# Performance work log

Hardware: AMD Instinct MI355X
Metric: run time of the kernel (lower is better)

Reference implementation:

```python
import jax, jax.numpy as jnp
import numpy as np

D_MODEL = 2048
DOWN = 512
UP = 1024
NUM_HEADS = 16
ROPE_DIM = 64
BS = 16
SEQ = 512
BASE = 10000.0
HEAD_DIM = D_MODEL // NUM_HEADS          # 128 (used only in the softmax scale)
V_HEAD_DIM = UP // NUM_HEADS             # 64


def _linear(x, W, b):
    # torch nn.Linear: y = x @ W.T + b, W shape (out, in)
    return x @ W.T + b


def _rope(x, num_heads, rope_dim):
    # Faithful to source RotaryEmbedding, including the swapped sin/cos caches:
    #   cos_pos = sin(pos*theta), sin_pos = cos(pos*theta)
    bs, L, _ = x.shape
    q = x.reshape(bs, L, num_heads, rope_dim).transpose(0, 2, 1, 3)  # (bs,h,L,d)
    theta = 1.0 / (BASE ** (jnp.arange(0, rope_dim, 2, dtype=jnp.float32) / rope_dim))
    ang = jnp.arange(L, dtype=jnp.float32)[:, None] * theta[None, :]   # (L, d/2)
    cos_pos = jnp.repeat(jnp.sin(ang), 2, axis=-1)  # (L, d) -- source quirk
    sin_pos = jnp.repeat(jnp.cos(ang), 2, axis=-1)
    q2 = jnp.stack([-q[..., 1::2], q[..., ::2]], axis=-1).reshape(bs, num_heads, L, rope_dim)
    return q * cos_pos + q2 * sin_pos


def setup_inputs() -> dict:
    key = jax.random.key(0)
    ks = jax.random.split(key, 18)
    s = 0.02
    d = {
        "h": jax.random.normal(ks[0], (BS, SEQ, D_MODEL), jnp.float32),
        "W_down_kv": jax.random.normal(ks[1], (DOWN, D_MODEL), jnp.float32) * s,
        "b_down_kv": jnp.zeros((DOWN,), jnp.float32),
        "W_up_k": jax.random.normal(ks[2], (UP, DOWN), jnp.float32) * s,
        "b_up_k": jnp.zeros((UP,), jnp.float32),
        "W_up_v": jax.random.normal(ks[3], (UP, DOWN), jnp.float32) * s,
        "b_up_v": jnp.zeros((UP,), jnp.float32),
        "W_down_q": jax.random.normal(ks[4], (DOWN, D_MODEL), jnp.float32) * s,
        "b_down_q": jnp.zeros((DOWN,), jnp.float32),
        "W_up_q": jax.random.normal(ks[5], (UP, DOWN), jnp.float32) * s,
        "b_up_q": jnp.zeros((UP,), jnp.float32),
        "W_qr": jax.random.normal(ks[6], (ROPE_DIM * NUM_HEADS, DOWN), jnp.float32) * s,
        "b_qr": jnp.zeros((ROPE_DIM * NUM_HEADS,), jnp.float32),
        "W_kr": jax.random.normal(ks[7], (ROPE_DIM, D_MODEL), jnp.float32) * s,
        "b_kr": jnp.zeros((ROPE_DIM,), jnp.float32),
        "W_fc": jax.random.normal(ks[8], (D_MODEL, NUM_HEADS * V_HEAD_DIM), jnp.float32) * s,
        "b_fc": jnp.zeros((D_MODEL,), jnp.float32),
    }
    return d


def reference(h, W_down_kv, b_down_kv, W_up_k, b_up_k, W_up_v, b_up_v,
              W_down_q, b_down_q, W_up_q, b_up_q, W_qr, b_qr,
              W_kr, b_kr, W_fc, b_fc):
    bs, L, _ = h.shape
    # low-rank KV path
    c_kv = _linear(h, W_down_kv, b_down_kv)             # (bs,L,down)
    k_c = _linear(c_kv, W_up_k, b_up_k)                 # (bs,L,up)
    v_c = _linear(c_kv, W_up_v, b_up_v)                 # (bs,L,up)
    # low-rank Q path
    c_q = _linear(h, W_down_q, b_down_q)                # (bs,L,down)
    q_c = _linear(c_q, W_up_q, b_up_q)                  # (bs,L,up)
    # rope (decoupled) path
    q_r = _rope(_linear(c_q, W_qr, b_qr), NUM_HEADS, ROPE_DIM)  # (bs,H,L,rope)
    k_r = _rope(_linear(h, W_kr, b_kr), 1, ROPE_DIM)            # (bs,1,L,rope)

    q_c = q_c.reshape(bs, L, NUM_HEADS, -1).transpose(0, 2, 1, 3)  # (bs,H,L,64)
    q = jnp.concatenate([q_c, q_r], axis=-1)                        # (bs,H,L,128)
    k_c = k_c.reshape(bs, L, NUM_HEADS, -1).transpose(0, 2, 1, 3)
    k_r = jnp.broadcast_to(k_r, (bs, NUM_HEADS, L, ROPE_DIM))       # shared across heads
    k = jnp.concatenate([k_c, k_r], axis=-1)

    scale = 1.0 / jnp.sqrt(jnp.float32(HEAD_DIM + ROPE_DIM))  # sqrt(192), per source
    scores = jnp.einsum('bhqd,bhkd->bhqk', q, k) * scale
    attn = jax.nn.softmax(scores, axis=-1)  # dropout is identity in eval mode

    v = v_c.reshape(bs, L, NUM_HEADS, V_HEAD_DIM).transpose(0, 2, 1, 3)
    out = jnp.einsum('bhqk,bhkd->bhqd', attn, v)
    out = out.transpose(0, 2, 1, 3).reshape(bs, L, -1)   # (bs,L,H*v_head_dim)
    return _linear(out, W_fc, b_fc)                      # (bs,L,d_model)
```

## Files before the change

kernel.cpp:

```cpp
#include <hip/hip_runtime.h>
#include <hip/hip_bf16.h>

typedef __bf16 bf16x8 __attribute__((ext_vector_type(8)));
typedef float f32x4 __attribute__((ext_vector_type(4)));
using u16 = unsigned short;
using u32 = unsigned int;

__device__ __forceinline__ float bf2f(u16 v) {
    unsigned int u = (unsigned int)v << 16;
    float f; __builtin_memcpy(&f, &u, 4); return f;
}
__device__ __forceinline__ u16 f2bf(float f) {
    unsigned int u; __builtin_memcpy(&u, &f, 4);
    u += 0x7FFFu + ((u >> 16) & 1u);
    return (u16)(u >> 16);
}

struct Cvt9 {
    const float* src[9];
    u16* dst[9];
    int end[9];
};
__global__ __launch_bounds__(256) void cvt_all(Cvt9 d, int total)
{
    int c = blockIdx.x * 256 + threadIdx.x;
    if (c >= total) return;
    int seg = 0;
    while (c >= d.end[seg]) ++seg;
    int local = c - (seg ? d.end[seg - 1] : 0);
    const float* s = d.src[seg] + (size_t)local * 8;
    float4 f0 = *(const float4*)s;
    float4 f1 = *(const float4*)(s + 4);
    u16 tmp[8] = { f2bf(f0.x), f2bf(f0.y), f2bf(f0.z), f2bf(f0.w),
                   f2bf(f1.x), f2bf(f1.y), f2bf(f1.z), f2bf(f1.w) };
    *(uint4*)(d.dst[seg] + (size_t)local * 8) = *(const uint4*)tmp;
}

struct Cpy7 {
    const float* src[7];
    float* dst[7];
    int end[7];
};
__global__ __launch_bounds__(256) void copy_f32(Cpy7 d, int total)
{
    int c = blockIdx.x * 256 + threadIdx.x;
    if (c >= total) return;
    int seg = 0;
    while (c >= d.end[seg]) ++seg;
    int local = c - (seg ? d.end[seg - 1] : 0);
    d.dst[seg][local] = d.src[seg][local];
}

template<bool CF>
__global__ __launch_bounds__(256) void gemm_v5(
    const u16* __restrict__ A0, const u16* __restrict__ B0, void* __restrict__ C0, const float* __restrict__ e0,
    const u16* __restrict__ A1, const u16* __restrict__ B1, void* __restrict__ C1, const float* __restrict__ e1,
    int ysplit, int lda, int ldb, int ldc, int N, int K)
{
    __shared__ __align__(16) u16 As[3][128 * 32];
    __shared__ __align__(16) u16 Bs[3][128 * 32];

    const int t = threadIdx.x;
    const int lane = t & 63;
    const int w = t >> 6;
    const int wm = w >> 1, wn = w & 1;
    const int l16 = lane & 15, quad = lane >> 4;
    const int m0 = blockIdx.x * 128;

    const u16* A; const u16* B; void* Cv; const float* bias; int yl;
    if ((int)blockIdx.y < ysplit) { A = A0; B = B0; Cv = C0; bias = e0; yl = blockIdx.y; }
    else                          { A = A1; B = B1; Cv = C1; bias = e1; yl = blockIdx.y - ysplit; }
    const int n0 = yl * 128;

    const int sub  = lane >> 2;
    const int slot = lane & 3;
    const int agc  = slot ^ ((sub >> 1) & 3);
    const int sfr  = (l16 >> 1) & 3;

    f32x4 acc[4][4];
#pragma unroll
    for (int i = 0; i < 4; ++i)
#pragma unroll
        for (int j = 0; j < 4; ++j) acc[i][j] = (f32x4){0.f, 0.f, 0.f, 0.f};

    auto STAGE = [&](int buf, int k0) {
#pragma unroll
        for (int c = 0; c < 2; ++c) {
            const int rr = w * 32 + c * 16;
            const u16* ga = A + (size_t)(m0 + rr + sub) * lda + k0 + agc * 8;
            __builtin_amdgcn_global_load_lds(
                (const __attribute__((address_space(1))) u32*)ga,
                (__attribute__((address_space(3))) u32*)&As[buf][rr * 32], 16, 0, 0);
            const u16* gb = B + (size_t)(n0 + rr + sub) * ldb + k0 + agc * 8;
            __builtin_amdgcn_global_load_lds(
                (const __attribute__((address_space(1))) u32*)gb,
                (__attribute__((address_space(3))) u32*)&Bs[buf][rr * 32], 16, 0, 0);
        }
    };

    const int nt = K >> 5;
    STAGE(0, 0);
    STAGE(1, 32);
    int cur = 0;
    for (int tt = 0; tt < nt; ++tt) {
        int pre = cur + 2; if (pre >= 3) pre -= 3;
        if (tt + 2 < nt) {
            STAGE(pre, (tt + 2) << 5);
            asm volatile("s_waitcnt vmcnt(8)");
        } else if (tt + 1 < nt) {
            asm volatile("s_waitcnt vmcnt(4)");
        } else {
            asm volatile("s_waitcnt vmcnt(0)");
        }
        __builtin_amdgcn_sched_barrier(0);
        __builtin_amdgcn_s_barrier();
        __builtin_amdgcn_sched_barrier(0);

        const u16* Ab = As[cur];
        const u16* Bb = Bs[cur];
        bf16x8 af[4], bfr[4];
#pragma unroll
        for (int i = 0; i < 4; ++i)
            af[i] = *(const bf16x8*)&Ab[(wm * 64 + i * 16 + l16) * 32 + (quad ^ sfr) * 8];
#pragma unroll
        for (int j = 0; j < 4; ++j)
            bfr[j] = *(const bf16x8*)&Bb[(wn * 64 + j * 16 + l16) * 32 + (quad ^ sfr) * 8];
#pragma unroll
        for (int i = 0; i < 4; ++i)
#pragma unroll
            for (int j = 0; j < 4; ++j)
                acc[i][j] = __builtin_amdgcn_mfma_f32_16x16x32_bf16(bfr[j], af[i], acc[i][j], 0, 0, 0);

        __builtin_amdgcn_s_barrier();
        __builtin_amdgcn_sched_barrier(0);
        cur += 1; if (cur >= 3) cur -= 3;
    }

#pragma unroll
    for (int i = 0; i < 4; ++i) {
        const int row = m0 + wm * 64 + i * 16 + l16;
#pragma unroll
        for (int j = 0; j < 4; ++j) {
            const int colb = n0 + wn * 64 + j * 16 + quad * 4;
            if (colb >= N) continue;
            float4 bv = *(const float4*)&bias[colb];
            float v0 = acc[i][j][0] + bv.x;
            float v1 = acc[i][j][1] + bv.y;
            float v2 = acc[i][j][2] + bv.z;
            float v3 = acc[i][j][3] + bv.w;
            if (CF) {
                float4 out = { v0, v1, v2, v3 };
                *(float4*)((float*)Cv + (size_t)row * ldc + colb) = out;
            } else {
                u16 p[4] = { f2bf(v0), f2bf(v1), f2bf(v2), f2bf(v3) };
                *(uint2*)((u16*)Cv + (size_t)row * ldc + colb) = *(const uint2*)p;
            }
        }
    }
}

__global__ void rope_inplace(u16* __restrict__ buf, int ld, int col0, int ppr, int total)
{
    int idx = blockIdx.x * 256 + threadIdx.x;
    if (idx >= total) return;
    int row = idx / ppr;
    int pi  = idx - row * ppr;
    int grp = pi >> 5;
    int i   = pi & 31;
    int pos = row & 511;
    float theta = __expf(-(float)i * 0.2878231366242558f);
    float ang = (float)pos * theta;
    float s = sinf(ang), c = cosf(ang);
    size_t base = (size_t)row * ld + col0 + grp * 64 + 2 * i;
    float x0 = bf2f(buf[base]);
    float x1 = bf2f(buf[base + 1]);
    buf[base]     = f2bf(x0 * s - x1 * c);
    buf[base + 1] = f2bf(x1 * s + x0 * c);
}

__global__ __launch_bounds__(256) void attn_kernel(
    const u16* __restrict__ q_src,
    const u16* __restrict__ kv_src,
    const u16* __restrict__ kr_src,
    u16* __restrict__ o_dst, int ldo)
{
    __shared__ __align__(16) u16 Ks[64 * 136];
    __shared__ __align__(16) u16 Vt[64 * 72];
    __shared__ __align__(16) u16 Ps[64 * 72];

    const int t = threadIdx.x;
    const int lane = t & 63;
    const int w = t >> 6;
    const int l16 = lane & 15, quad = lane >> 4;

    const int id   = blockIdx.x;
    const int xcd  = id & 7;
    const int qt   = (id >> 3) & 7;
    const int panel = xcd + ((id >> 6) << 3);
    const int h = panel & 15;
    const int b = panel >> 4;
    const int qrow0 = b * 512 + qt * 64;
    const int krow_base = b * 512;

    bf16x8 aq[4];
    {
        const u16* qrow = q_src + (size_t)(qrow0 + w * 16 + l16) * 2048;
#pragma unroll
        for (int ks = 0; ks < 4; ++ks) {
            int col = ks * 32 + quad * 8;
            const u16* src = (col < 64) ? qrow + h * 64 + col
                                        : qrow + 1024 + h * 64 + (col - 64);
            aq[ks] = *(const bf16x8*)src;
        }
    }

    const int colK = (t & 15) * 8;
    const int r0k  = t >> 4;
    const u16* kbase; int kstr;
    if (colK < 64) { kbase = kv_src + h * 64 + colK;        kstr = 2048; }
    else           { kbase = kr_src + 1024 + (colK - 64);   kstr = 1088; }
    u16* kw = &Ks[r0k * 136 + colK];

    const int v00 = (t & 7) * 8;
    const int r0v = t >> 3;
    const u16* vbase = kv_src + 1024 + h * 64 + v00;
    const int rotA = (r0v + v00) & 63;
    const int rotB = (r0v + 32 + v00) & 63;
    u16* vwA = &Vt[v00 * 72 + rotA];
    u16* vwB = &Vt[v00 * 72 + rotB];

    auto LOADT = [&](int krow0, uint4& K0, uint4& K1, uint4& K2, uint4& K3,
                     uint4& V0, uint4& V1) {
        K0 = *(const uint4*)(kbase + (size_t)(krow0 + r0k     ) * kstr);
        K1 = *(const uint4*)(kbase + (size_t)(krow0 + r0k + 16) * kstr);
        K2 = *(const uint4*)(kbase + (size_t)(krow0 + r0k + 32) * kstr);
        K3 = *(const uint4*)(kbase + (size_t)(krow0 + r0k + 48) * kstr);
        V0 = *(const uint4*)(vbase + (size_t)(krow0 + r0v     ) * 2048);
        V1 = *(const uint4*)(vbase + (size_t)(krow0 + r0v + 32) * 2048);
    };
    auto WRITET = [&](const uint4& K0, const uint4& K1, const uint4& K2, const uint4& K3,
                      const uint4& V0, const uint4& V1) {
        *(uint4*)(kw)            = K0;
        *(uint4*)(kw + 16 * 136) = K1;
        *(uint4*)(kw + 32 * 136) = K2;
        *(uint4*)(kw + 48 * 136) = K3;
        u16 ta[8], tb[8];
        __builtin_memcpy(ta, &V0, 16);
        __builtin_memcpy(tb, &V1, 16);
#pragma unroll
        for (int j2 = 0; j2 < 8; ++j2) { vwA[j2 * 72] = ta[j2]; vwB[j2 * 72] = tb[j2]; }
    };

    float m2[4], l_run[4];
    f32x4 o[4];
#pragma unroll
    for (int r = 0; r < 4; ++r) { m2[r] = -1e30f; l_run[r] = 0.f; }
#pragma unroll
    for (int n = 0; n < 4; ++n) o[n] = (f32x4){0.f, 0.f, 0.f, 0.f};

    const float C = 0.10411756f;
    const int Rp = (64 - (quad << 4)) & 48;
    const int Rr = (64 - ((l16 >> 2) << 4)) & 48;

    uint4 kA0, kA1, kA2, kA3, vA0, vA1;
    uint4 kB0, kB1, kB2, kB3, vB0, vB1;
    LOADT(krow_base, kA0, kA1, kA2, kA3, vA0, vA1);

    for (int kt = 0; kt < 8; ++kt) {
        __builtin_amdgcn_s_barrier();
        __builtin_amdgcn_sched_barrier(0);
        if ((kt & 1) == 0) {
            WRITET(kA0, kA1, kA2, kA3, vA0, vA1);
            if (kt < 7) LOADT(krow_base + (kt + 1) * 64, kB0, kB1, kB2, kB3, vB0, vB1);
        } else {
            WRITET(kB0, kB1, kB2, kB3, vB0, vB1);
            if (kt < 7) LOADT(krow_base + (kt + 1) * 64, kA0, kA1, kA2, kA3, vA0, vA1);
        }
        asm volatile("s_waitcnt lgkmcnt(0)");
        __builtin_amdgcn_sched_barrier(0);
        __builtin_amdgcn_s_barrier();
        __builtin_amdgcn_sched_barrier(0);

        f32x4 s[4];
#pragma unroll
        for (int n = 0; n < 4; ++n) s[n] = (f32x4){0.f, 0.f, 0.f, 0.f};
#pragma unroll
        for (int ks = 0; ks < 4; ++ks) {
#pragma unroll
            for (int n = 0; n < 4; ++n) {
                bf16x8 bk = *(const bf16x8*)&Ks[(n * 16 + l16) * 136 + ks * 32 + quad * 8];
                s[n] = __builtin_amdgcn_mfma_f32_16x16x32_bf16(aq[ks], bk, s[n], 0, 0, 0);
            }
        }

        float mx[4], alpha[4], rs[4];
#pragma unroll
        for (int r = 0; r < 4; ++r)
            mx[r] = fmaxf(fmaxf(s[0][r], s[1][r]), fmaxf(s[2][r], s[3][r]));
#pragma unroll
        for (int d = 1; d < 16; d <<= 1)
#pragma unroll
            for (int r = 0; r < 4; ++r)
                mx[r] = fmaxf(mx[r], __shfl_xor(mx[r], d));
#pragma unroll
        for (int r = 0; r < 4; ++r) {
            float mnew = fmaxf(m2[r], mx[r] * C);
            alpha[r] = __builtin_amdgcn_exp2f(m2[r] - mnew);
            m2[r] = mnew;
            rs[r] = 0.f;
#pragma unroll
            for (int n = 0; n < 4; ++n) {
                float pv = __builtin_amdgcn_exp2f(__builtin_fmaf(s[n][r], C, -mnew));
                s[n][r] = pv;
                rs[r] += pv;
            }
        }
#pragma unroll
        for (int d = 1; d < 16; d <<= 1)
#pragma unroll
            for (int r = 0; r < 4; ++r)
                rs[r] += __shfl_xor(rs[r], d);
#pragma unroll
        for (int r = 0; r < 4; ++r) {
            l_run[r] = l_run[r] * alpha[r] + rs[r];
#pragma unroll
            for (int n = 0; n < 4; ++n) o[n][r] *= alpha[r];
        }

#pragma unroll
        for (int n = 0; n < 4; ++n) {
            int pc = (n * 16 + l16 + Rp) & 63;
#pragma unroll
            for (int r = 0; r < 4; ++r)
                Ps[(w * 16 + quad * 4 + r) * 72 + pc] = f2bf(s[n][r]);
        }

#pragma unroll
        for (int kk = 0; kk < 2; ++kk) {
            bf16x8 ap = *(const bf16x8*)&Ps[(w * 16 + l16) * 72 + ((kk * 32 + quad * 8 + Rr) & 63)];
#pragma unroll
            for (int n = 0; n < 4; ++n) {
                bf16x8 bv = *(const bf16x8*)&Vt[(n * 16 + l16) * 72
                              + ((kk * 32 + quad * 8 + n * 16 + (l16 & 8)) & 63)];
                o[n] = __builtin_amdgcn_mfma_f32_16x16x32_bf16(ap, bv, o[n], 0, 0, 0);
            }
        }
    }

#pragma unroll
    for (int r = 0; r < 4; ++r) {
        float inv = 1.0f / l_run[r];
        int row = qrow0 + w * 16 + quad * 4 + r;
#pragma unroll
        for (int n = 0; n < 4; ++n) {
            int col = h * 64 + n * 16 + l16;
            o_dst[(size_t)row * ldo + col] = f2bf(o[n][r] * inv);
        }
    }
}

extern "C" void kernel_launch(void* const* d_in, const int* in_sizes, int n_in,
                              void* d_out, int out_size, void* d_ws, size_t ws_size,
                              hipStream_t stream)
{
    const float* h    = (const float*)d_in[0];
    const float* Wdkv = (const float*)d_in[1];
    const float* bdkv = (const float*)d_in[2];
    const float* Wuk  = (const float*)d_in[3];
    const float* buk  = (const float*)d_in[4];
    const float* Wuv  = (const float*)d_in[5];
    const float* buv  = (const float*)d_in[6];
    const float* Wdq  = (const float*)d_in[7];
    const float* bdq  = (const float*)d_in[8];
    const float* Wuq  = (const float*)d_in[9];
    const float* buq  = (const float*)d_in[10];
    const float* Wqr  = (const float*)d_in[11];
    const float* bqr  = (const float*)d_in[12];
    const float* Wkr  = (const float*)d_in[13];
    const float* bkr  = (const float*)d_in[14];
    const float* Wfc  = (const float*)d_in[15];
    const float* bfc  = (const float*)d_in[16];

    char* ws = (char*)d_ws;
    u16* out1   = (u16*)ws;
    u16* hbf    = (u16*)(ws + 17825792);
    u16* out2a  = hbf;
    u16* out2b  = (u16*)(ws + 51380224);
    u16* w1     = (u16*)(ws + 84934656);
    u16* w2a    = (u16*)(ws + 89653248);
    u16* w2b    = (u16*)(ws + 91750400);
    u16* wfc    = (u16*)(ws + 93847552);
    float* bias_s1 = (float*)(ws + 98041856);
    float* bias_2  = (float*)(ws + 98046208);

    Cvt9 cd;
    const float* srcs[9] = { h, Wdkv, Wdq, Wkr, Wuk, Wuv, Wuq, Wqr, Wfc };
    u16* dsts[9] = { hbf, w1, w1 + 512 * 2048, w1 + 1024 * 2048,
                     w2a, w2a + 1024 * 512, w2b, w2b + 1024 * 512, wfc };
    int cnts[9] = { 2097152, 131072, 131072, 16384, 65536, 65536, 65536, 65536, 262144 };
    int acc2 = 0;
    for (int i = 0; i < 9; ++i) { cd.src[i] = srcs[i]; cd.dst[i] = dsts[i]; acc2 += cnts[i]; cd.end[i] = acc2; }
    cvt_all<<<(acc2 + 255) / 256, 256, 0, stream>>>(cd, acc2);
    hipMemsetAsync(w1 + 1088 * 2048, 0, 64 * 2048 * sizeof(u16), stream);

    Cpy7 bc;
    const float* bs[7] = { bdkv, bdq, bkr, buk, buv, buq, bqr };
    float* bd[7] = { bias_s1, bias_s1 + 512, bias_s1 + 1024,
                     bias_2, bias_2 + 1024, bias_2 + 2048, bias_2 + 3072 };
    int bn[7] = { 512, 512, 64, 1024, 1024, 1024, 1024 };
    int bacc = 0;
    for (int i = 0; i < 7; ++i) { bc.src[i] = bs[i]; bc.dst[i] = bd[i]; bacc += bn[i]; bc.end[i] = bacc; }
    copy_f32<<<(bacc + 255) / 256, 256, 0, stream>>>(bc, bacc);

    gemm_v5<false><<<dim3(64, 9), 256, 0, stream>>>(
        hbf, w1, out1, bias_s1,
        hbf, w1, out1, bias_s1, 9, 2048, 2048, 1088, 1088, 2048);
    rope_inplace<<<1024, 256, 0, stream>>>(out1, 1088, 1024, 32, 8192 * 32);

    gemm_v5<false><<<dim3(64, 32), 256, 0, stream>>>(
        out1,       w2a, out2a, bias_2,
        out1 + 512, w2b, out2b, bias_2 + 2048, 16, 1088, 512, 2048, 2048, 512);
    rope_inplace<<<16384, 256, 0, stream>>>(out2b, 2048, 1024, 512, 8192 * 512);

    attn_kernel<<<2048, 256, 0, stream>>>(out2b, out2a, out1, out1, 1088);

    gemm_v5<true><<<dim3(64, 16), 256, 0, stream>>>(
        out1, wfc, d_out, bfc,
        out1, wfc, d_out, bfc, 16, 1088, 1024, 2048, 2048, 1024);
}
```

Measured before the change: 434.9 us.

## Transpose QK MFMA operands to make softmax row-local and XOR-swizzle P buffer

The attention kernel swaps the QK^T MFMA operands so each lane holds scores for a single query row. The row max and row sum then need only two cross-quad shuffles instead of four-step butterflies over four rows, and alpha and 1/l are broadcast to the output layout via __shfl. P is now written as packed 32-bit bf16 pairs into an XOR-swizzled shared buffer instead of scalar 16-bit stores. Several sched_barrier fences are also removed in the GEMM and attention loops to give the compiler more scheduling freedom, at the risk of worse instruction interleaving.

```diff
diff --git a/kernel.cpp b/kernel.cpp
--- a/kernel.cpp
+++ b/kernel.cpp
@@ -52,7 +52,7 @@
 }
 
 template<bool CF>
-__global__ __launch_bounds__(256) void gemm_v5(
+__global__ __launch_bounds__(256) void gemm_v6(
     const u16* __restrict__ A0, const u16* __restrict__ B0, void* __restrict__ C0, const float* __restrict__ e0,
     const u16* __restrict__ A1, const u16* __restrict__ B1, void* __restrict__ C1, const float* __restrict__ e1,
     int ysplit, int lda, int ldb, int ldc, int N, int K)
@@ -112,9 +112,7 @@
         } else {
             asm volatile("s_waitcnt vmcnt(0)");
         }
-        __builtin_amdgcn_sched_barrier(0);
         __builtin_amdgcn_s_barrier();
-        __builtin_amdgcn_sched_barrier(0);
 
         const u16* Ab = As[cur];
         const u16* Bb = Bs[cur];
@@ -124,7 +122,7 @@
             af[i] = *(const bf16x8*)&Ab[(wm * 64 + i * 16 + l16) * 32 + (quad ^ sfr) * 8];
 #pragma unroll
         for (int j = 0; j < 4; ++j)
-            bfr[j] = *(const bf16x8*)&Bb[(wn * 64 + j * 16 + l16) * 32 + (quad ^ sfr) * 8];
+            bfr[j] = *(const bf16x8*)&Bs[cur][(wn * 64 + j * 16 + l16) * 32 + (quad ^ sfr) * 8];
 #pragma unroll
         for (int i = 0; i < 4; ++i)
 #pragma unroll
@@ -132,8 +130,8 @@
                 acc[i][j] = __builtin_amdgcn_mfma_f32_16x16x32_bf16(bfr[j], af[i], acc[i][j], 0, 0, 0);
 
         __builtin_amdgcn_s_barrier();
-        __builtin_amdgcn_sched_barrier(0);
         cur += 1; if (cur >= 3) cur -= 3;
+        (void)Bb;
     }
 
 #pragma unroll
@@ -192,6 +190,7 @@
     const int lane = t & 63;
     const int w = t >> 6;
     const int l16 = lane & 15, quad = lane >> 4;
+    const int a7 = l16 & 7;
 
     const int id   = blockIdx.x;
     const int xcd  = id & 7;
@@ -251,16 +250,12 @@
         for (int j2 = 0; j2 < 8; ++j2) { vwA[j2 * 72] = ta[j2]; vwB[j2 * 72] = tb[j2]; }
     };
 
-    float m2[4], l_run[4];
+    float m2 = -1e30f, l_run = 0.f;
     f32x4 o[4];
 #pragma unroll
-    for (int r = 0; r < 4; ++r) { m2[r] = -1e30f; l_run[r] = 0.f; }
-#pragma unroll
     for (int n = 0; n < 4; ++n) o[n] = (f32x4){0.f, 0.f, 0.f, 0.f};
 
     const float C = 0.10411756f;
-    const int Rp = (64 - (quad << 4)) & 48;
-    const int Rr = (64 - ((l16 >> 2) << 4)) & 48;
 
     uint4 kA0, kA1, kA2, kA3, vA0, vA1;
     uint4 kB0, kB1, kB2, kB3, vB0, vB1;
@@ -268,7 +263,6 @@
 
     for (int kt = 0; kt < 8; ++kt) {
         __builtin_amdgcn_s_barrier();
-        __builtin_amdgcn_sched_barrier(0);
         if ((kt & 1) == 0) {
             WRITET(kA0, kA1, kA2, kA3, vA0, vA1);
             if (kt < 7) LOADT(krow_base + (kt + 1) * 64, kB0, kB1, kB2, kB3, vB0, vB1);
@@ -279,7 +273,6 @@
         asm volatile("s_waitcnt lgkmcnt(0)");
         __builtin_amdgcn_sched_barrier(0);
         __builtin_amdgcn_s_barrier();
-        __builtin_amdgcn_sched_barrier(0);
 
         f32x4 s[4];
 #pragma unroll
@@ -289,55 +282,58 @@
 #pragma unroll
             for (int n = 0; n < 4; ++n) {
                 bf16x8 bk = *(const bf16x8*)&Ks[(n * 16 + l16) * 136 + ks * 32 + quad * 8];
-                s[n] = __builtin_amdgcn_mfma_f32_16x16x32_bf16(aq[ks], bk, s[n], 0, 0, 0);
+                s[n] = __builtin_amdgcn_mfma_f32_16x16x32_bf16(bk, aq[ks], s[n], 0, 0, 0);
             }
         }
 
-        float mx[4], alpha[4], rs[4];
-#pragma unroll
-        for (int r = 0; r < 4; ++r)
-            mx[r] = fmaxf(fmaxf(s[0][r], s[1][r]), fmaxf(s[2][r], s[3][r]));
-#pragma unroll
-        for (int d = 1; d < 16; d <<= 1)
-#pragma unroll
-            for (int r = 0; r < 4; ++r)
-                mx[r] = fmaxf(mx[r], __shfl_xor(mx[r], d));
-#pragma unroll
-        for (int r = 0; r < 4; ++r) {
-            float mnew = fmaxf(m2[r], mx[r] * C);
-            alpha[r] = __builtin_amdgcn_exp2f(m2[r] - mnew);
-            m2[r] = mnew;
-            rs[r] = 0.f;
-#pragma unroll
-            for (int n = 0; n < 4; ++n) {
+        float mx = fmaxf(fmaxf(s[0][0], s[0][1]), fmaxf(s[0][2], s[0][3]));
+#pragma unroll
+        for (int n = 1; n < 4; ++n)
+            mx = fmaxf(mx, fmaxf(fmaxf(s[n][0], s[n][1]), fmaxf(s[n][2], s[n][3])));
+        mx = fmaxf(mx, __shfl_xor(mx, 16));
+        mx = fmaxf(mx, __shfl_xor(mx, 32));
+
+        float mnew = fmaxf(m2, mx * C);
+        float alpha = __builtin_amdgcn_exp2f(m2 - mnew);
+        m2 = mnew;
+        float rs = 0.f;
+#pragma unroll
+        for (int n = 0; n < 4; ++n)
+#pragma unroll
+            for (int r = 0; r < 4; ++r) {
                 float pv = __builtin_amdgcn_exp2f(__builtin_fmaf(s[n][r], C, -mnew));
                 s[n][r] = pv;
-                rs[r] += pv;
+                rs += pv;
             }
-        }
-#pragma unroll
-        for (int d = 1; d < 16; d <<= 1)
-#pragma unroll
-            for (int r = 0; r < 4; ++r)
-                rs[r] += __shfl_xor(rs[r], d);
-#pragma unroll
-        for (int r = 0; r < 4; ++r) {
-            l_run[r] = l_run[r] * alpha[r] + rs[r];
-#pragma unroll
-            for (int n = 0; n < 4; ++n) o[n][r] *= alpha[r];
-        }
-
-#pragma unroll
-        for (int n = 0; n < 4; ++n) {
-            int pc = (n * 16 + l16 + Rp) & 63;
-#pragma unroll
-            for (int r = 0; r < 4; ++r)
-                Ps[(w * 16 + quad * 4 + r) * 72 + pc] = f2bf(s[n][r]);
+        rs += __shfl_xor(rs, 16);
+        rs += __shfl_xor(rs, 32);
+        l_run = l_run * alpha + rs;
+
+        float aO[4];
+#pragma unroll
+        for (int r = 0; r < 4; ++r) aO[r] = __shfl(alpha, quad * 4 + r);
+#pragma unroll
+        for (int n = 0; n < 4; ++n)
+#pragma unroll
+            for (int r = 0; r < 4; ++r) o[n][r] *= aO[r];
+
+        {
+            u16* prow = &Ps[(w * 16 + l16) * 72];
+#pragma unroll
+            for (int n = 0; n < 4; ++n) {
+                int cb = n * 16 + quad * 4;
+                int pc = (((cb >> 3) ^ a7) << 3) + (cb & 7);
+                u32 p0 = (u32)f2bf(s[n][0]) | ((u32)f2bf(s[n][1]) << 16);
+                u32 p1 = (u32)f2bf(s[n][2]) | ((u32)f2bf(s[n][3]) << 16);
+                *(u32*)&prow[pc]     = p0;
+                *(u32*)&prow[pc + 2] = p1;
+            }
         }
 
 #pragma unroll
         for (int kk = 0; kk < 2; ++kk) {
-            bf16x8 ap = *(const bf16x8*)&Ps[(w * 16 + l16) * 72 + ((kk * 32 + quad * 8 + Rr) & 63)];
+            int gb = 4 * kk + quad;
+            bf16x8 ap = *(const bf16x8*)&Ps[(w * 16 + l16) * 72 + ((gb ^ a7) << 3)];
 #pragma unroll
             for (int n = 0; n < 4; ++n) {
                 bf16x8 bv = *(const bf16x8*)&Vt[(n * 16 + l16) * 72
@@ -347,14 +343,15 @@
         }
     }
 
+    float inv = 1.0f / l_run;
 #pragma unroll
     for (int r = 0; r < 4; ++r) {
-        float inv = 1.0f / l_run[r];
+        float invO = __shfl(inv, quad * 4 + r);
         int row = qrow0 + w * 16 + quad * 4 + r;
 #pragma unroll
         for (int n = 0; n < 4; ++n) {
             int col = h * 64 + n * 16 + l16;
-            o_dst[(size_t)row * ldo + col] = f2bf(o[n][r] * inv);
+            o_dst[(size_t)row * ldo + col] = f2bf(o[n][r] * invO);
         }
     }
 }
@@ -412,19 +409,19 @@
     for (int i = 0; i < 7; ++i) { bc.src[i] = bs[i]; bc.dst[i] = bd[i]; bacc += bn[i]; bc.end[i] = bacc; }
     copy_f32<<<(bacc + 255) / 256, 256, 0, stream>>>(bc, bacc);
 
-    gemm_v5<false><<<dim3(64, 9), 256, 0, stream>>>(
+    gemm_v6<false><<<dim3(64, 9), 256, 0, stream>>>(
         hbf, w1, out1, bias_s1,
         hbf, w1, out1, bias_s1, 9, 2048, 2048, 1088, 1088, 2048);
     rope_inplace<<<1024, 256, 0, stream>>>(out1, 1088, 1024, 32, 8192 * 32);
 
-    gemm_v5<false><<<dim3(64, 32), 256, 0, stream>>>(
+    gemm_v6<false><<<dim3(64, 32), 256, 0, stream>>>(
         out1,       w2a, out2a, bias_2,
         out1 + 512, w2b, out2b, bias_2 + 2048, 16, 1088, 512, 2048, 2048, 512);
     rope_inplace<<<16384, 256, 0, stream>>>(out2b, 2048, 1024, 512, 8192 * 512);
 
     attn_kernel<<<2048, 256, 0, stream>>>(out2b, out2a, out1, out1, 1088);
 
-    gemm_v5<true><<<dim3(64, 16), 256, 0, stream>>>(
+    gemm_v6<true><<<dim3(64, 16), 256, 0, stream>>>(
         out1, wfc, d_out, bfc,
         out1, wfc, d_out, bfc, 16, 1088, 1024, 2048, 2048, 1024);
 }
```

Result: faster. 424.2 us (-2.5%).
